# Kernel optimization log

Hardware: AMD Instinct MI355X
Metric: run time of the kernel (lower is better)

## Reference

```python
import jax, jax.numpy as jnp
import numpy as np

K, M, N = 8, 1024, 1024  # bits, in_features, out_features (nf)
B_, S_ = 4, 2048

def setup_inputs() -> dict:
    key = jax.random.key(0)
    k1, k2, k3, k4 = jax.random.split(key, 4)
    x = jax.random.normal(k1, (B_, S_, M), dtype=jnp.float32)
    # per-bit +/-1 sign matrices, stored as float (module casts int8 -> x.dtype)
    binary = jnp.where(jax.random.normal(k2, (K, M, N)) > 0, 1.0, -1.0).astype(jnp.float32)
    # positive per-bit, per-output-channel scales (sup decomposition yields positives)
    scale = jax.random.uniform(k3, (K, 1, N), dtype=jnp.float32, minval=0.01, maxval=1.0)
    bias = jax.random.normal(k4, (N,), dtype=jnp.float32)
    return {"x": x, "binary": binary, "scale": scale, "bias": bias}

def reference(x, binary, scale, bias):
    size_out = x.shape[:-1] + (N,)
    x2 = x.reshape(-1, x.shape[-1])                 # [T, m]
    # k separate dense matmuls against +/-1 matrices: [k, T, n]
    xk = jnp.einsum('tm,kmn->ktn', x2, binary)
    out = jnp.sum(xk * scale, axis=0)               # per-bit scale then sum over bits
    out = out + bias
    return out.reshape(size_out)
```

## Files before the change

kernel.cpp:

```cpp
#include <hip/hip_runtime.h>
#include <cstdint>

#define TDIM 8192
#define MDIM 1024
#define NDIM 1024
#define KBITS 8
#define BK 64
#define BT 128
#define BN 128
#define NTILES (MDIM / BK)

typedef __bf16 bf16x8 __attribute__((ext_vector_type(8)));
typedef float f32x4 __attribute__((ext_vector_type(4)));

#define GAS(p) ((__attribute__((address_space(1))) void*)(uintptr_t)(p))
#define LAS(p) ((__attribute__((address_space(3))) void*)(uintptr_t)(p))

__device__ __forceinline__ unsigned f2bf(float f) {
    union { float f; unsigned u; } v; v.f = f;
    unsigned r = v.u + 0x7fffu + ((v.u >> 16) & 1u);
    return r >> 16;
}

__global__ __launch_bounds__(256) void prep_kernel(const float* __restrict__ x,
                                                   unsigned short* __restrict__ xb,
                                                   const float* __restrict__ binary,
                                                   const float* __restrict__ scale,
                                                   unsigned short* __restrict__ wtrp) {
    __shared__ float tile[32][33];
    const int tid = threadIdx.x;
    if (blockIdx.x >= 1024) {
        size_t idx = ((size_t)(blockIdx.x - 1024) * 256 + tid) * 8;
        float4 a = *(const float4*)(x + idx);
        float4 b = *(const float4*)(x + idx + 4);
        uint4 o;
        o.x = f2bf(a.x) | (f2bf(a.y) << 16);
        o.y = f2bf(a.z) | (f2bf(a.w) << 16);
        o.z = f2bf(b.x) | (f2bf(b.y) << 16);
        o.w = f2bf(b.z) | (f2bf(b.w) << 16);
        *(uint4*)(xb + idx) = o;
        return;
    }
    const int n0 = (blockIdx.x & 31) * 32;
    const int m0 = (blockIdx.x >> 5) * 32;
    const int r = tid >> 3;
    const int cn = (tid & 7) * 4;
    f32x4 acc = {0.f, 0.f, 0.f, 0.f};
#pragma unroll
    for (int k = 0; k < KBITS; ++k) {
        f32x4 v = *(const f32x4*)(binary + ((size_t)k * MDIM + m0 + r) * NDIM + n0 + cn);
        f32x4 s = *(const f32x4*)(scale + (size_t)k * NDIM + n0 + cn);
        acc += v * s;
    }
#pragma unroll
    for (int e = 0; e < 4; ++e) tile[cn + e][r] = acc[e];
    __syncthreads();
    const int rn = tid >> 3;
    const int cm = (tid & 7) * 4;
    const int n = n0 + rn;
    const int m = m0 + cm;
    ushort4 o4;
    o4.x = (unsigned short)f2bf(tile[rn][cm + 0]);
    o4.y = (unsigned short)f2bf(tile[rn][cm + 1]);
    o4.z = (unsigned short)f2bf(tile[rn][cm + 2]);
    o4.w = (unsigned short)f2bf(tile[rn][cm + 3]);
    *(ushort4*)(wtrp + ((size_t)(n >> 4) * 128 + (m >> 3)) * 128 + (n & 15) * 8 + (m & 7)) = o4;
}

__global__ __launch_bounds__(256, 3) void gemm_kernel(const unsigned short* __restrict__ xb,
                                                      const unsigned short* __restrict__ wtrp,
                                                      const float* __restrict__ bias,
                                                      float* __restrict__ out) {
    constexpr int ASZ = BT * BK;
    __shared__ __attribute__((aligned(16))) unsigned short lds[2 * ASZ];

    const int tid = threadIdx.x;
    const int lane = tid & 63;
    const int wv = tid >> 6;
    const int wm = wv >> 1;
    const int wn = wv & 1;
    const int lrow = lane & 15;
    const int q = lane >> 4;

    const int t0 = blockIdx.x * BT;
    const int n0 = blockIdx.y * BN;
    const int nt0 = blockIdx.y * (BN / 16);

    const unsigned short* srcA[4];
    int dstA[4];
#pragma unroll
    for (int j = 0; j < 4; ++j) {
        int s = tid + j * 256;
        int r = s >> 3;
        int g = (s & 7) ^ (r & 7);
        srcA[j] = xb + (size_t)(t0 + r) * MDIM + g * 8;
        dstA[j] = s * 8;
    }

    int a_off[2][4];
#pragma unroll
    for (int h = 0; h < 2; ++h)
#pragma unroll
        for (int i = 0; i < 4; ++i) {
            int m = wm * 64 + i * 16 + lrow;
            a_off[h][i] = (m * 8 + ((h * 4 + q) ^ (m & 7))) * 8;
        }

    const unsigned short* bbase[4];
#pragma unroll
    for (int i = 0; i < 4; ++i)
        bbase[i] = wtrp + (size_t)(nt0 + wn * 4 + i) * 16384 + q * 128 + lrow * 8;

    f32x4 acc[4][4];
    const f32x4 zero = {0.f, 0.f, 0.f, 0.f};
#pragma unroll
    for (int i = 0; i < 4; ++i)
#pragma unroll
        for (int j = 0; j < 4; ++j) acc[i][j] = zero;

    auto stageA = [&](int bufsel, int t) {
        unsigned short* bb = lds + bufsel * ASZ;
        const int k0 = t * BK;
#pragma unroll
        for (int j = 0; j < 4; ++j)
            __builtin_amdgcn_global_load_lds(GAS(srcA[j] + k0), LAS(bb + dstA[j]), 16, 0, 0);
    };

    stageA(0, 0);
    __syncthreads();

#pragma unroll
    for (int t = 0; t < NTILES; ++t) {
        const int cur = t & 1;

        bf16x8 bfr0[4], bfr1[4];
#pragma unroll
        for (int i = 0; i < 4; ++i) bfr0[i] = *(const bf16x8*)(bbase[i] + (t * 2 + 0) * 512);
#pragma unroll
        for (int i = 0; i < 4; ++i) bfr1[i] = *(const bf16x8*)(bbase[i] + (t * 2 + 1) * 512);

        if (t + 1 < NTILES) stageA(cur ^ 1, t + 1);

        const unsigned short* base = lds + cur * ASZ;
#pragma unroll
        for (int h = 0; h < 2; ++h) {
            bf16x8 af[4];
#pragma unroll
            for (int i = 0; i < 4; ++i) af[i] = *(const bf16x8*)(base + a_off[h][i]);
            __builtin_amdgcn_s_setprio(1);
#pragma unroll
            for (int i = 0; i < 4; ++i)
#pragma unroll
                for (int j = 0; j < 4; ++j)
                    acc[i][j] = __builtin_amdgcn_mfma_f32_16x16x32_bf16(
                        af[i], (h == 0) ? bfr0[j] : bfr1[j], acc[i][j], 0, 0, 0);
            __builtin_amdgcn_s_setprio(0);
        }

        if (t + 1 < NTILES) __syncthreads();
    }

#pragma unroll
    for (int j = 0; j < 4; ++j) {
        const int n = n0 + wn * 64 + j * 16 + lrow;
        const float bv = bias[n];
#pragma unroll
        for (int i = 0; i < 4; ++i) {
            const int tb = t0 + wm * 64 + i * 16 + q * 4;
#pragma unroll
            for (int r = 0; r < 4; ++r) {
                out[(size_t)(tb + r) * NDIM + n] = acc[i][j][r] + bv;
            }
        }
    }
}

extern "C" void kernel_launch(void* const* d_in, const int* in_sizes, int n_in,
                              void* d_out, int out_size, void* d_ws, size_t ws_size,
                              hipStream_t stream) {
    const float* x      = (const float*)d_in[0];
    const float* binary = (const float*)d_in[1];
    const float* scale  = (const float*)d_in[2];
    const float* bias   = (const float*)d_in[3];
    float* out = (float*)d_out;

    unsigned short* xb   = (unsigned short*)d_ws;
    unsigned short* wtrp = xb + (size_t)TDIM * MDIM;

    prep_kernel<<<1024 + 4096, 256, 0, stream>>>(x, xb, binary, scale, wtrp);
    gemm_kernel<<<dim3(TDIM / BT, NDIM / BN), 256, 0, stream>>>(xb, wtrp, bias, out);
}
```

Measured before the change: 124.7 us.

## Fuse fp32-to-bf16 conversion of activations into GEMM A-tile load

Removes the separate pass that converted x to bf16 in workspace and instead streams fp32 x directly into LDS, converting to bf16 in registers right before the MFMA. This eliminates a full write and re-read of the bf16 activation copy. In exchange, LDS usage doubles (64KB per block), occupancy hint drops from 3 to 2 blocks, and each tile needs twice as many global-to-LDS loads and LDS reads plus per-element conversion work in the inner loop.

```diff
diff --git a/kernel.cpp b/kernel.cpp
--- a/kernel.cpp
+++ b/kernel.cpp
@@ -22,25 +22,11 @@
     return r >> 16;
 }
 
-__global__ __launch_bounds__(256) void prep_kernel(const float* __restrict__ x,
-                                                   unsigned short* __restrict__ xb,
-                                                   const float* __restrict__ binary,
-                                                   const float* __restrict__ scale,
-                                                   unsigned short* __restrict__ wtrp) {
+__global__ __launch_bounds__(256) void wfold_kernel(const float* __restrict__ binary,
+                                                    const float* __restrict__ scale,
+                                                    unsigned short* __restrict__ wtrp) {
     __shared__ float tile[32][33];
     const int tid = threadIdx.x;
-    if (blockIdx.x >= 1024) {
-        size_t idx = ((size_t)(blockIdx.x - 1024) * 256 + tid) * 8;
-        float4 a = *(const float4*)(x + idx);
-        float4 b = *(const float4*)(x + idx + 4);
-        uint4 o;
-        o.x = f2bf(a.x) | (f2bf(a.y) << 16);
-        o.y = f2bf(a.z) | (f2bf(a.w) << 16);
-        o.z = f2bf(b.x) | (f2bf(b.y) << 16);
-        o.w = f2bf(b.z) | (f2bf(b.w) << 16);
-        *(uint4*)(xb + idx) = o;
-        return;
-    }
     const int n0 = (blockIdx.x & 31) * 32;
     const int m0 = (blockIdx.x >> 5) * 32;
     const int r = tid >> 3;
@@ -67,12 +53,19 @@
     *(ushort4*)(wtrp + ((size_t)(n >> 4) * 128 + (m >> 3)) * 128 + (n & 15) * 8 + (m & 7)) = o4;
 }
 
-__global__ __launch_bounds__(256, 3) void gemm_kernel(const unsigned short* __restrict__ xb,
+__device__ __forceinline__ bf16x8 cvt8(f32x4 lo, f32x4 hi) {
+    bf16x8 r;
+    r[0] = (__bf16)lo[0]; r[1] = (__bf16)lo[1]; r[2] = (__bf16)lo[2]; r[3] = (__bf16)lo[3];
+    r[4] = (__bf16)hi[0]; r[5] = (__bf16)hi[1]; r[6] = (__bf16)hi[2]; r[7] = (__bf16)hi[3];
+    return r;
+}
+
+__global__ __launch_bounds__(256, 2) void gemm_kernel(const float* __restrict__ x,
                                                       const unsigned short* __restrict__ wtrp,
                                                       const float* __restrict__ bias,
                                                       float* __restrict__ out) {
     constexpr int ASZ = BT * BK;
-    __shared__ __attribute__((aligned(16))) unsigned short lds[2 * ASZ];
+    __shared__ __attribute__((aligned(16))) float lds[2 * ASZ];
 
     const int tid = threadIdx.x;
     const int lane = tid & 63;
@@ -86,24 +79,27 @@
     const int n0 = blockIdx.y * BN;
     const int nt0 = blockIdx.y * (BN / 16);
 
-    const unsigned short* srcA[4];
-    int dstA[4];
+    const float* srcA[8];
+    int dstA[8];
 #pragma unroll
-    for (int j = 0; j < 4; ++j) {
+    for (int j = 0; j < 8; ++j) {
         int s = tid + j * 256;
-        int r = s >> 3;
-        int g = (s & 7) ^ (r & 7);
-        srcA[j] = xb + (size_t)(t0 + r) * MDIM + g * 8;
-        dstA[j] = s * 8;
+        int r = s >> 4;
+        int g = (s & 15) ^ (r & 15);
+        srcA[j] = x + (size_t)(t0 + r) * MDIM + g * 4;
+        dstA[j] = s * 4;
     }
 
-    int a_off[2][4];
+    int a_lo[2][4], a_hi[2][4];
 #pragma unroll
     for (int h = 0; h < 2; ++h)
 #pragma unroll
         for (int i = 0; i < 4; ++i) {
             int m = wm * 64 + i * 16 + lrow;
-            a_off[h][i] = (m * 8 + ((h * 4 + q) ^ (m & 7))) * 8;
+            int e = m & 15;
+            int gk = 8 * h + 2 * q;
+            a_lo[h][i] = m * 64 + ((gk    ) ^ e) * 4;
+            a_hi[h][i] = m * 64 + ((gk + 1) ^ e) * 4;
         }
 
     const unsigned short* bbase[4];
@@ -119,10 +115,10 @@
         for (int j = 0; j < 4; ++j) acc[i][j] = zero;
 
     auto stageA = [&](int bufsel, int t) {
-        unsigned short* bb = lds + bufsel * ASZ;
+        float* bb = lds + bufsel * ASZ;
         const int k0 = t * BK;
 #pragma unroll
-        for (int j = 0; j < 4; ++j)
+        for (int j = 0; j < 8; ++j)
             __builtin_amdgcn_global_load_lds(GAS(srcA[j] + k0), LAS(bb + dstA[j]), 16, 0, 0);
     };
 
@@ -141,12 +137,16 @@
 
         if (t + 1 < NTILES) stageA(cur ^ 1, t + 1);
 
-        const unsigned short* base = lds + cur * ASZ;
+        const float* base = lds + cur * ASZ;
 #pragma unroll
         for (int h = 0; h < 2; ++h) {
             bf16x8 af[4];
 #pragma unroll
-            for (int i = 0; i < 4; ++i) af[i] = *(const bf16x8*)(base + a_off[h][i]);
+            for (int i = 0; i < 4; ++i) {
+                f32x4 lo = *(const f32x4*)(base + a_lo[h][i]);
+                f32x4 hi = *(const f32x4*)(base + a_hi[h][i]);
+                af[i] = cvt8(lo, hi);
+            }
             __builtin_amdgcn_s_setprio(1);
 #pragma unroll
             for (int i = 0; i < 4; ++i)
@@ -184,9 +184,8 @@
     const float* bias   = (const float*)d_in[3];
     float* out = (float*)d_out;
 
-    unsigned short* xb   = (unsigned short*)d_ws;
-    unsigned short* wtrp = xb + (size_t)TDIM * MDIM;
+    unsigned short* wtrp = (unsigned short*)d_ws;
 
-    prep_kernel<<<1024 + 4096, 256, 0, stream>>>(x, xb, binary, scale, wtrp);
-    gemm_kernel<<<dim3(TDIM / BT, NDIM / BN), 256, 0, stream>>>(xb, wtrp, bias, out);
+    wfold_kernel<<<1024, 256, 0, stream>>>(binary, scale, wtrp);
+    gemm_kernel<<<dim3(TDIM / BT, NDIM / BN), 256, 0, stream>>>(x, wtrp, bias, out);
 }
```

After: 127.3 us. 1.02x slower.
